# Performance work log

Measured on AMD Instinct MI355X. Metric: run time of the kernel, lower is better.

Reference implementation:

```python
import jax, jax.numpy as jnp
import numpy as np

ALPHA = 0.2  # LeakyReLU negative slope


def setup_inputs() -> dict:
    key = jax.random.key(0)
    ks = jax.random.split(key, 6)
    B, N, F_in, F_out, H = 16, 1024, 256, 256, 8
    h = jax.random.normal(ks[0], (B, N, F_in), dtype=jnp.float32)
    # Per-head Linear W: weight [F_out, F_in] + bias [F_out], stacked over heads
    W = jax.random.normal(ks[1], (H, F_out, F_in), dtype=jnp.float32) * (1.414 / np.sqrt(F_in))
    bW = jax.random.normal(ks[2], (H, F_out), dtype=jnp.float32) * 0.01
    # Per-head Linear A: weight [1, 2*F_out] split into a1 (acts on Whi) and a2 (acts on Whj), bias bA [1]
    a1 = jax.random.normal(ks[3], (H, F_out), dtype=jnp.float32) * (1.414 / np.sqrt(2 * F_out))
    a2 = jax.random.normal(ks[4], (H, F_out), dtype=jnp.float32) * (1.414 / np.sqrt(2 * F_out))
    bA = jax.random.normal(ks[5], (H,), dtype=jnp.float32) * 0.01
    return {"h": h, "W": W, "bW": bW, "a1": a1, "a2": a2, "bA": bA}


def reference(h, W, bW, a1, a2, bA):
    # h: [B,N,F_in], W: [H,F_out,F_in]
    B, N, _ = h.shape
    H, F_out, _ = W.shape
    Wh = jnp.einsum('bnf,hof->bhno', h, W) + bW[None, :, None, :]  # [B,H,N,F_out]
    # Additive score e_ij = a1.Wh_i + a2.Wh_j + bA  (decomposed; avoids N x N x 2F concat)
    ei = jnp.einsum('bhno,ho->bhn', Wh, a1)  # contribution of row node i
    ej = jnp.einsum('bhno,ho->bhn', Wh, a2)  # contribution of col node j
    e = ei[:, :, :, None] + ej[:, :, None, :] + bA[None, :, None, None]  # [B,H,N,N]
    e = jnp.where(e > 0, e, ALPHA * e)  # LeakyReLU
    att = jax.nn.softmax(e, axis=-1)  # softmax over neighbors j (dropout = identity in eval)
    aWh = jnp.einsum('bhij,bhjo->bhio', att, Wh)  # [B,H,N,F_out]
    out = jax.nn.relu(aWh)  # last=False branch
    out = out.transpose(0, 2, 1, 3).reshape(B, N, H * F_out)  # concat heads on feature dim
    return jax.nn.sigmoid(out)
```

## Files before the change

kernel.cpp:

```cpp
#include <hip/hip_runtime.h>


#define L2E 1.442695041f

typedef _Float16 half8 __attribute__((ext_vector_type(8)));
typedef __fp16 fp16x2 __attribute__((ext_vector_type(2)));
typedef float floatx4 __attribute__((ext_vector_type(4)));

#if __has_builtin(__builtin_amdgcn_exp2f)
#define EXP2F(x) __builtin_amdgcn_exp2f(x)
#else
#define EXP2F(x) exp2f(x)
#endif

static __device__ inline unsigned int pack2(float a, float b) {
    fp16x2 h = __builtin_amdgcn_cvt_pkrtz(a, b);
    return __builtin_bit_cast(unsigned int, h);
}

static __device__ inline int swz(int row, int c) {
    return (row << 6) + ((((c) ^ (row >> 1)) & 3) << 4);
}

__global__ __launch_bounds__(512, 2) void wh_kernel(
    const float* __restrict__ hin, const float* __restrict__ W,
    const float* __restrict__ bW, _Float16* __restrict__ WhT,
    const float* __restrict__ a1, const float* __restrict__ a2,
    float* __restrict__ ei, float* __restrict__ ej)
{
    const int bnt  = blockIdx.x;
    const int head = blockIdx.y;
    const int t    = threadIdx.x;
    const int wave = t >> 6, lane = t & 63;
    const int l15 = lane & 15, quad = lane >> 4;

    __shared__ char smem[24576];
    _Float16* As = (_Float16*)smem;
    _Float16* Bs = (_Float16*)(smem + 16384);
    float* bWs  = (float*)smem;
    float* a1s  = (float*)(smem + 1024);
    float* a2s  = (float*)(smem + 2048);
    float* red1 = (float*)(smem + 3072);
    float* red2 = (float*)(smem + 3584);

    const int bn0 = bnt * 128;
    floatx4 acc[4][4];
#pragma unroll
    for (int a = 0; a < 4; a++)
#pragma unroll
        for (int b = 0; b < 4; b++) acc[a][b] = (floatx4)0.0f;

    const int wm = (wave & 3) * 4;
    const int wn = (wave >> 2) * 4;

    const int ar = t >> 1, ah = t & 1;
    const int br = t >> 2, bc = t & 3;
    const float* Wrow = W + (size_t)(head * 256 + ar) * 256 + ah * 16;
    const float* hrow = hin + (size_t)(bn0 + br) * 256 + bc * 8;

    float4 pa0, pa1, pa2, pa3, pb0, pb1;
    {
        const float4* p4 = (const float4*)Wrow;
        pa0 = p4[0]; pa1 = p4[1]; pa2 = p4[2]; pa3 = p4[3];
        const float4* q4 = (const float4*)hrow;
        pb0 = q4[0]; pb1 = q4[1];
    }

    for (int f0 = 0; f0 < 256; f0 += 32) {
        __syncthreads();
        *(uint4*)((char*)As + swz(ar, 2 * ah)) =
            make_uint4(pack2(pa0.x, pa0.y), pack2(pa0.z, pa0.w),
                       pack2(pa1.x, pa1.y), pack2(pa1.z, pa1.w));
        *(uint4*)((char*)As + swz(ar, 2 * ah + 1)) =
            make_uint4(pack2(pa2.x, pa2.y), pack2(pa2.z, pa2.w),
                       pack2(pa3.x, pa3.y), pack2(pa3.z, pa3.w));
        *(uint4*)((char*)Bs + swz(br, bc)) =
            make_uint4(pack2(pb0.x, pb0.y), pack2(pb0.z, pb0.w),
                       pack2(pb1.x, pb1.y), pack2(pb1.z, pb1.w));
        if (f0 < 224) {
            const float4* p4 = (const float4*)(Wrow + f0 + 32);
            pa0 = p4[0]; pa1 = p4[1]; pa2 = p4[2]; pa3 = p4[3];
            const float4* q4 = (const float4*)(hrow + f0 + 32);
            pb0 = q4[0]; pb1 = q4[1];
        }
        __syncthreads();
        half8 af[4], bf[4];
#pragma unroll
        for (int a = 0; a < 4; a++)
            af[a] = *(const half8*)((char*)As + swz((wm + a) * 16 + l15, quad));
#pragma unroll
        for (int b = 0; b < 4; b++)
            bf[b] = *(const half8*)((char*)Bs + swz((wn + b) * 16 + l15, quad));
#pragma unroll
        for (int a = 0; a < 4; a++)
#pragma unroll
            for (int b = 0; b < 4; b++)
                acc[a][b] = __builtin_amdgcn_mfma_f32_16x16x32_f16(af[a], bf[b], acc[a][b], 0, 0, 0);
    }

    __syncthreads();
    if (t < 256) {
        bWs[t] = bW[head * 256 + t];
        a1s[t] = a1[head * 256 + t];
        a2s[t] = a2[head * 256 + t];
    }
    if (t < 128) { red1[t] = 0.f; red2[t] = 0.f; }
    __syncthreads();

    const int bidx = bn0 >> 10;
    const int nbase = bn0 & 1023;
#pragma unroll
    for (int b = 0; b < 4; b++) {
        const int bnl = (wn + b) * 16 + l15;
        const int n = nbase + bnl;
        float p1 = 0.f, p2 = 0.f;
#pragma unroll
        for (int a = 0; a < 4; a++) {
#pragma unroll
            for (int r = 0; r < 4; r++) {
                int o = (wm + a) * 16 + quad * 4 + r;
                float v = acc[a][b][r] + bWs[o];
                WhT[(((size_t)(bidx * 8 + head) * 256 + o) << 10) + n] = (_Float16)v;
                p1 = fmaf(v, a1s[o], p1);
                p2 = fmaf(v, a2s[o], p2);
            }
        }
        atomicAdd(&red1[bnl], p1);
        atomicAdd(&red2[bnl], p2);
    }
    __syncthreads();
    if (t < 128) {
        const size_t idx = (size_t)(bidx * 8 + head) * 1024 + nbase + t;
        ei[idx] = red1[t];
        ej[idx] = red2[t];
    }
}

__global__ __launch_bounds__(512, 2) void pv_kernel(
    const _Float16* __restrict__ WhT, const float* __restrict__ ei,
    const float* __restrict__ ej, const float* __restrict__ bA,
    float* __restrict__ out)
{
    const int bh = blockIdx.x;
    const int it = blockIdx.y;
    const int b = bh >> 3, head = bh & 7;
    const int t = threadIdx.x;
    const int wave = t >> 6, lane = t & 63;
    const int l15 = lane & 15, quad = lane >> 4;

    __shared__ char smem[29248];
    _Float16* Ap = (_Float16*)smem;
    _Float16* Bp = (_Float16*)(smem + 8192);
    float* ejs  = (float*)(smem + 24576);
    float* lns  = (float*)(smem + 28672);
    float* wred = (float*)(smem + 29184);

    const float* ejrow = ej + bh * 1024;
    float v0 = ejrow[t] * L2E, v1 = ejrow[t + 512] * L2E;
    ejs[t] = v0; ejs[t + 512] = v1;
    float mx = fmaxf(v0, v1);
#pragma unroll
    for (int m = 32; m; m >>= 1) mx = fmaxf(mx, __shfl_xor(mx, m, 64));
    if (lane == 0) wred[wave] = mx;
    __syncthreads();
    float ejmax = wred[0];
#pragma unroll
    for (int w = 1; w < 8; w++) ejmax = fmaxf(ejmax, wred[w]);

    const int i0 = it * 128;
    const int prow = t >> 2, pc = t & 3;
    const float cip = (ei[bh * 1024 + i0 + prow] + bA[head]) * L2E;
    const float tmv = cip + ejmax;
    const float nm = -fmaxf(tmv, 0.2f * tmv);

    const int wr = t >> 1, wh2 = t & 1;
    const _Float16* wrow = WhT + ((size_t)bh << 18) + ((size_t)wr << 10) + wh2 * 16;

    floatx4 acc[2][8], accl[2];
#pragma unroll
    for (int a = 0; a < 2; a++) {
        accl[a] = (floatx4)0.0f;
#pragma unroll
        for (int c = 0; c < 8; c++) acc[a][c] = (floatx4)0.0f;
    }
    const int wm = (wave >> 1) * 2;
    const int wn = (wave & 1) * 8;
    const bool doL = (wn == 0);
    const half8 ones = {1, 1, 1, 1, 1, 1, 1, 1};

    uint4 w0, w1;
    { const uint4* s = (const uint4*)wrow; w0 = s[0]; w1 = s[1]; }

    for (int j0 = 0; j0 < 1024; j0 += 32) {
        __syncthreads();
        {
            const float* ejp = ejs + j0 + pc * 8;
            float p[8];
#pragma unroll
            for (int u = 0; u < 8; u++) {
                float e = cip + ejp[u];
                float lr = fmaxf(e, 0.2f * e);
                p[u] = EXP2F(lr + nm);
            }
            *(uint4*)((char*)Ap + swz(prow, pc)) =
                make_uint4(pack2(p[0], p[1]), pack2(p[2], p[3]),
                           pack2(p[4], p[5]), pack2(p[6], p[7]));
        }
        *(uint4*)((char*)Bp + swz(wr, 2 * wh2)) = w0;
        *(uint4*)((char*)Bp + swz(wr, 2 * wh2 + 1)) = w1;
        if (j0 < 992) {
            const uint4* s = (const uint4*)(wrow + j0 + 32);
            w0 = s[0]; w1 = s[1];
        }
        __syncthreads();
        half8 af[2], bf[8];
#pragma unroll
        for (int a = 0; a < 2; a++)
            af[a] = *(const half8*)((char*)Ap + swz((wm + a) * 16 + l15, quad));
#pragma unroll
        for (int c = 0; c < 8; c++)
            bf[c] = *(const half8*)((char*)Bp + swz((wn + c) * 16 + l15, quad));
        if (doL) {
#pragma unroll
            for (int a = 0; a < 2; a++)
                accl[a] = __builtin_amdgcn_mfma_f32_16x16x32_f16(af[a], ones, accl[a], 0, 0, 0);
        }
#pragma unroll
        for (int a = 0; a < 2; a++)
#pragma unroll
            for (int c = 0; c < 8; c++)
                acc[a][c] = __builtin_amdgcn_mfma_f32_16x16x32_f16(af[a], bf[c], acc[a][c], 0, 0, 0);
    }

    __syncthreads();
    if (doL && l15 == 0) {
#pragma unroll
        for (int a = 0; a < 2; a++)
#pragma unroll
            for (int r = 0; r < 4; r++)
                lns[(wm + a) * 16 + quad * 4 + r] = accl[a][r];
    }
    __syncthreads();

    float rinv[2][4];
#pragma unroll
    for (int a = 0; a < 2; a++)
#pragma unroll
        for (int r = 0; r < 4; r++)
            rinv[a][r] = 1.0f / lns[(wm + a) * 16 + quad * 4 + r];

#pragma unroll
    for (int a = 0; a < 2; a++) {
#pragma unroll
        for (int c = 0; c < 8; c++) {
            int o = (wn + c) * 16 + l15;
#pragma unroll
            for (int r = 0; r < 4; r++) {
                int i = i0 + (wm + a) * 16 + quad * 4 + r;
                float v = acc[a][c][r] * rinv[a][r];
                float rl = fmaxf(v, 0.0f);
                float y = 1.0f / (1.0f + EXP2F(-rl * L2E));
                out[((size_t)(b * 1024 + i) << 11) + head * 256 + o] = y;
            }
        }
    }
}

extern "C" void kernel_launch(void* const* d_in, const int* in_sizes, int n_in,
                              void* d_out, int out_size, void* d_ws, size_t ws_size,
                              hipStream_t stream)
{
    const float* h  = (const float*)d_in[0];
    const float* W  = (const float*)d_in[1];
    const float* bW = (const float*)d_in[2];
    const float* a1 = (const float*)d_in[3];
    const float* a2 = (const float*)d_in[4];
    const float* bA = (const float*)d_in[5];
    float* out = (float*)d_out;

    char* ws = (char*)d_ws;
    _Float16* WhT = (_Float16*)ws;
    float* ei = (float*)(ws + 67108864);
    float* ej = (float*)(ws + 67108864 + 524288);

    hipLaunchKernelGGL(wh_kernel, dim3(128, 8), dim3(512), 0, stream,
                       h, W, bW, WhT, a1, a2, ei, ej);
    hipLaunchKernelGGL(pv_kernel, dim3(128, 8), dim3(512), 0, stream,
                       WhT, ei, ej, bA, out);
}
```

Before: 329.0 us.

## Widen PV K-tile to 64, rebalance wave tiling, replace LDS atomics with shuffles

New measurement: 322.0 us. 1.02x faster.

```diff
diff --git a/kernel.cpp b/kernel.cpp
--- a/kernel.cpp
+++ b/kernel.cpp
@@ -20,6 +20,9 @@
 
 static __device__ inline int swz(int row, int c) {
     return (row << 6) + ((((c) ^ (row >> 1)) & 3) << 4);
+}
+static __device__ inline int swz128(int row, int c) {
+    return (row << 7) + ((((c) ^ row) & 7) << 4);
 }
 
 __global__ __launch_bounds__(512, 2) void wh_kernel(
@@ -37,11 +40,11 @@
     __shared__ char smem[24576];
     _Float16* As = (_Float16*)smem;
     _Float16* Bs = (_Float16*)(smem + 16384);
-    float* bWs  = (float*)smem;
-    float* a1s  = (float*)(smem + 1024);
-    float* a2s  = (float*)(smem + 2048);
-    float* red1 = (float*)(smem + 3072);
-    float* red2 = (float*)(smem + 3584);
+    float* bWs   = (float*)smem;
+    float* a1s   = (float*)(smem + 1024);
+    float* a2s   = (float*)(smem + 2048);
+    float* part1 = (float*)(smem + 3072);
+    float* part2 = (float*)(smem + 5120);
 
     const int bn0 = bnt * 128;
     floatx4 acc[4][4];
@@ -104,11 +107,12 @@
         a1s[t] = a1[head * 256 + t];
         a2s[t] = a2[head * 256 + t];
     }
-    if (t < 128) { red1[t] = 0.f; red2[t] = 0.f; }
     __syncthreads();
 
     const int bidx = bn0 >> 10;
     const int nbase = bn0 & 1023;
+    const int g = wave >> 2;
+    const int wmw = wave & 3;
 #pragma unroll
     for (int b = 0; b < 4; b++) {
         const int bnl = (wn + b) * 16 + l15;
@@ -125,14 +129,25 @@
                 p2 = fmaf(v, a2s[o], p2);
             }
         }
-        atomicAdd(&red1[bnl], p1);
-        atomicAdd(&red2[bnl], p2);
+        p1 += __shfl_xor(p1, 16, 64); p1 += __shfl_xor(p1, 32, 64);
+        p2 += __shfl_xor(p2, 16, 64); p2 += __shfl_xor(p2, 32, 64);
+        if (lane < 16) {
+            part1[g * 256 + wmw * 64 + b * 16 + lane] = p1;
+            part2[g * 256 + wmw * 64 + b * 16 + lane] = p2;
+        }
     }
     __syncthreads();
     if (t < 128) {
+        const int gg = t >> 6, r = t & 63;
+        float s1 = 0.f, s2 = 0.f;
+#pragma unroll
+        for (int w = 0; w < 4; w++) {
+            s1 += part1[gg * 256 + w * 64 + r];
+            s2 += part2[gg * 256 + w * 64 + r];
+        }
         const size_t idx = (size_t)(bidx * 8 + head) * 1024 + nbase + t;
-        ei[idx] = red1[t];
-        ej[idx] = red2[t];
+        ei[idx] = s1;
+        ej[idx] = s2;
     }
 }
 
@@ -148,12 +163,12 @@
     const int wave = t >> 6, lane = t & 63;
     const int l15 = lane & 15, quad = lane >> 4;
 
-    __shared__ char smem[29248];
+    __shared__ char smem[53824];
     _Float16* Ap = (_Float16*)smem;
-    _Float16* Bp = (_Float16*)(smem + 8192);
-    float* ejs  = (float*)(smem + 24576);
-    float* lns  = (float*)(smem + 28672);
-    float* wred = (float*)(smem + 29184);
+    _Float16* Bp = (_Float16*)(smem + 16384);
+    float* ejs  = (float*)(smem + 49152);
+    float* lns  = (float*)(smem + 53248);
+    float* wred = (float*)(smem + 53760);
 
     const float* ejrow = ej + bh * 1024;
     float v0 = ejrow[t] * L2E, v1 = ejrow[t + 512] * L2E;
@@ -168,91 +183,103 @@
     for (int w = 1; w < 8; w++) ejmax = fmaxf(ejmax, wred[w]);
 
     const int i0 = it * 128;
-    const int prow = t >> 2, pc = t & 3;
+    const int prow = t >> 2, pjb = (t & 3) * 16;
     const float cip = (ei[bh * 1024 + i0 + prow] + bA[head]) * L2E;
     const float tmv = cip + ejmax;
     const float nm = -fmaxf(tmv, 0.2f * tmv);
 
-    const int wr = t >> 1, wh2 = t & 1;
-    const _Float16* wrow = WhT + ((size_t)bh << 18) + ((size_t)wr << 10) + wh2 * 16;
-
-    floatx4 acc[2][8], accl[2];
-#pragma unroll
-    for (int a = 0; a < 2; a++) {
+    const int wr_ = t >> 1, hh = t & 1;
+    const _Float16* wrow = WhT + ((size_t)bh << 18) + ((size_t)wr_ << 10) + hh * 32;
+
+    floatx4 acc[4][4], accl[4];
+#pragma unroll
+    for (int a = 0; a < 4; a++) {
         accl[a] = (floatx4)0.0f;
 #pragma unroll
-        for (int c = 0; c < 8; c++) acc[a][c] = (floatx4)0.0f;
-    }
-    const int wm = (wave >> 1) * 2;
-    const int wn = (wave & 1) * 8;
-    const bool doL = (wn == 0);
+        for (int c = 0; c < 4; c++) acc[a][c] = (floatx4)0.0f;
+    }
+    const int wm = (wave >> 2) * 4;
+    const int wn = (wave & 3) * 4;
+    const bool doL = ((wave & 3) == 0);
     const half8 ones = {1, 1, 1, 1, 1, 1, 1, 1};
 
-    uint4 w0, w1;
-    { const uint4* s = (const uint4*)wrow; w0 = s[0]; w1 = s[1]; }
-
-    for (int j0 = 0; j0 < 1024; j0 += 32) {
+    uint4 w0, w1, w2, w3;
+    { const uint4* s = (const uint4*)wrow; w0 = s[0]; w1 = s[1]; w2 = s[2]; w3 = s[3]; }
+
+    for (int j0 = 0; j0 < 1024; j0 += 64) {
         __syncthreads();
         {
-            const float* ejp = ejs + j0 + pc * 8;
-            float p[8];
-#pragma unroll
-            for (int u = 0; u < 8; u++) {
+            const float* ejp = ejs + j0 + pjb;
+            float p[16];
+#pragma unroll
+            for (int u = 0; u < 16; u++) {
                 float e = cip + ejp[u];
                 float lr = fmaxf(e, 0.2f * e);
                 p[u] = EXP2F(lr + nm);
             }
-            *(uint4*)((char*)Ap + swz(prow, pc)) =
+            const int c0 = (t & 3) * 2;
+            *(uint4*)((char*)Ap + swz128(prow, c0)) =
                 make_uint4(pack2(p[0], p[1]), pack2(p[2], p[3]),
                            pack2(p[4], p[5]), pack2(p[6], p[7]));
-        }
-        *(uint4*)((char*)Bp + swz(wr, 2 * wh2)) = w0;
-        *(uint4*)((char*)Bp + swz(wr, 2 * wh2 + 1)) = w1;
-        if (j0 < 992) {
-            const uint4* s = (const uint4*)(wrow + j0 + 32);
-            w0 = s[0]; w1 = s[1];
+            *(uint4*)((char*)Ap + swz128(prow, c0 + 1)) =
+                make_uint4(pack2(p[8], p[9]), pack2(p[10], p[11]),
+                           pack2(p[12], p[13]), pack2(p[14], p[15]));
+        }
+        {
+            const int c0 = 4 * hh;
+            *(uint4*)((char*)Bp + swz128(wr_, c0))     = w0;
+            *(uint4*)((char*)Bp + swz128(wr_, c0 + 1)) = w1;
+            *(uint4*)((char*)Bp + swz128(wr_, c0 + 2)) = w2;
+            *(uint4*)((char*)Bp + swz128(wr_, c0 + 3)) = w3;
+        }
+        if (j0 < 960) {
+            const uint4* s = (const uint4*)(wrow + j0 + 64);
+            w0 = s[0]; w1 = s[1]; w2 = s[2]; w3 = s[3];
         }
         __syncthreads();
-        half8 af[2], bf[8];
-#pragma unroll
-        for (int a = 0; a < 2; a++)
-            af[a] = *(const half8*)((char*)Ap + swz((wm + a) * 16 + l15, quad));
-#pragma unroll
-        for (int c = 0; c < 8; c++)
-            bf[c] = *(const half8*)((char*)Bp + swz((wn + c) * 16 + l15, quad));
-        if (doL) {
-#pragma unroll
-            for (int a = 0; a < 2; a++)
-                accl[a] = __builtin_amdgcn_mfma_f32_16x16x32_f16(af[a], ones, accl[a], 0, 0, 0);
-        }
-#pragma unroll
-        for (int a = 0; a < 2; a++)
-#pragma unroll
-            for (int c = 0; c < 8; c++)
-                acc[a][c] = __builtin_amdgcn_mfma_f32_16x16x32_f16(af[a], bf[c], acc[a][c], 0, 0, 0);
+#pragma unroll
+        for (int kk = 0; kk < 2; kk++) {
+            half8 af[4], bf[4];
+#pragma unroll
+            for (int a = 0; a < 4; a++)
+                af[a] = *(const half8*)((char*)Ap + swz128((wm + a) * 16 + l15, kk * 4 + quad));
+#pragma unroll
+            for (int c = 0; c < 4; c++)
+                bf[c] = *(const half8*)((char*)Bp + swz128((wn + c) * 16 + l15, kk * 4 + quad));
+            if (doL) {
+#pragma unroll
+                for (int a = 0; a < 4; a++)
+                    accl[a] = __builtin_amdgcn_mfma_f32_16x16x32_f16(af[a], ones, accl[a], 0, 0, 0);
+            }
+#pragma unroll
+            for (int a = 0; a < 4; a++)
+#pragma unroll
+                for (int c = 0; c < 4; c++)
+                    acc[a][c] = __builtin_amdgcn_mfma_f32_16x16x32_f16(af[a], bf[c], acc[a][c], 0, 0, 0);
+        }
     }
 
     __syncthreads();
     if (doL && l15 == 0) {
 #pragma unroll
-        for (int a = 0; a < 2; a++)
+        for (int a = 0; a < 4; a++)
 #pragma unroll
             for (int r = 0; r < 4; r++)
                 lns[(wm + a) * 16 + quad * 4 + r] = accl[a][r];
     }
     __syncthreads();
 
-    float rinv[2][4];
-#pragma unroll
-    for (int a = 0; a < 2; a++)
+    float rinv[4][4];
+#pragma unroll
+    for (int a = 0; a < 4; a++)
 #pragma unroll
         for (int r = 0; r < 4; r++)
             rinv[a][r] = 1.0f / lns[(wm + a) * 16 + quad * 4 + r];
 
 #pragma unroll
-    for (int a = 0; a < 2; a++) {
-#pragma unroll
-        for (int c = 0; c < 8; c++) {
+    for (int a = 0; a < 4; a++) {
+#pragma unroll
+        for (int c = 0; c < 4; c++) {
             int o = (wn + c) * 16 + l15;
 #pragma unroll
             for (int r = 0; r < 4; r++) {
```
